# Kernel optimization log

Hardware: AMD Instinct MI355X
Metric: run time of the kernel (lower is better)

## Reference

```python
import jax, jax.numpy as jnp
import numpy as np
import math

B, T, D_MODEL, N_HEADS = 2, 2048, 2048, 16
D_HEAD = D_MODEL // N_HEADS
ROPE_THETA = 10000.0


def setup_inputs() -> dict:
    key = jax.random.key(0)
    ks = jax.random.split(key, 4)
    x = jax.random.normal(ks[0], (B, T, D_MODEL), dtype=jnp.float32)
    # causal mask: True = masked (matches torch masked_fill semantics)
    mask = jnp.triu(jnp.ones((T, T), dtype=bool), k=1)[None, None]  # [1,1,T,T]
    # rotary freqs: complex freqs_cis = exp(i * t * theta^(-2j/d)) -> cos/sin parts
    inv_freq = 1.0 / (ROPE_THETA ** (jnp.arange(0, D_HEAD, 2, dtype=jnp.float32) / D_HEAD))
    angles = jnp.arange(T, dtype=jnp.float32)[:, None] * inv_freq[None, :]  # [T, D_HEAD//2]
    freqs_cos = jnp.cos(angles)
    freqs_sin = jnp.sin(angles)
    s = 1.0 / math.sqrt(D_MODEL)
    Wqkv = jax.random.normal(ks[1], (D_MODEL, 3 * D_MODEL), dtype=jnp.float32) * s
    bqkv = jnp.zeros((3 * D_MODEL,), dtype=jnp.float32)
    Wproj = jax.random.normal(ks[2], (D_MODEL, D_MODEL), dtype=jnp.float32) * s
    bproj = jnp.zeros((D_MODEL,), dtype=jnp.float32)
    return {"x": x, "mask": mask, "freqs_cos": freqs_cos, "freqs_sin": freqs_sin,
            "Wqkv": Wqkv, "bqkv": bqkv, "Wproj": Wproj, "bproj": bproj}


def _rope(t, cos, sin):
    # t: [B,H,T,D]; cos/sin: [1,1,T,D//2]. Complex multiply on (even, odd) pairs.
    t2 = t.reshape(*t.shape[:-1], -1, 2)
    t_re, t_im = t2[..., 0], t2[..., 1]
    out_re = t_re * cos - t_im * sin
    out_im = t_re * sin + t_im * cos
    return jnp.stack([out_re, out_im], axis=-1).reshape(t.shape)


def reference(x, mask, freqs_cos, freqs_sin, Wqkv, bqkv, Wproj, bproj):
    Bb, Tt, C = x.shape
    qkv = x @ Wqkv + bqkv                                   # [B,T,3C]
    q, k, v = jnp.split(qkv, 3, axis=-1)
    def heads(t):
        return t.reshape(Bb, Tt, N_HEADS, D_HEAD).transpose(0, 2, 1, 3)  # [B,H,T,D]
    q, k, v = heads(q), heads(k), heads(v)
    cos = freqs_cos[None, None]                              # [1,1,T,D//2]
    sin = freqs_sin[None, None]
    q = _rope(q, cos, sin)
    k = _rope(k, cos, sin)
    att = jnp.einsum('bhqd,bhkd->bhqk', q, k) / math.sqrt(D_HEAD)
    att = jnp.where(mask, -jnp.inf, att)
    att = jax.nn.softmax(att, axis=-1)
    # attn_dropout is identity in eval mode
    out = jnp.einsum('bhqk,bhkd->bhqd', att, v)              # [B,H,T,D]
    out = out.transpose(0, 2, 1, 3).reshape(Bb, Tt, C)
    return (out @ Wproj + bproj, k, v)
```

## Files before the change

### kernel.cpp

```cpp
#include <hip/hip_runtime.h>
#include <hip/hip_bf16.h>

#define T_SEQ 2048
#define DM    2048
#define NH    16
#define DH    128
#define NBH   32
#define MROWS 4096

typedef __bf16 bf16x8 __attribute__((ext_vector_type(8)));
typedef __bf16 bf16x4 __attribute__((ext_vector_type(4)));
typedef float  f32x4  __attribute__((ext_vector_type(4)));

#define MFMA16 __builtin_amdgcn_mfma_f32_16x16x32_bf16

__device__ __forceinline__ void async_copy16(const void* g, void* l) {
  __builtin_amdgcn_global_load_lds((const __attribute__((address_space(1))) void*)g,
                                   (__attribute__((address_space(3))) void*)l, 16, 0, 0);
}


__global__ void cast_bf16_k(const float* __restrict__ x, __bf16* __restrict__ xb) {
  int i = (blockIdx.x * 256 + threadIdx.x) * 4;
  float4 v = *reinterpret_cast<const float4*>(x + i);
  bf16x4 o;
  o[0] = (__bf16)v.x; o[1] = (__bf16)v.y; o[2] = (__bf16)v.z; o[3] = (__bf16)v.w;
  *reinterpret_cast<bf16x4*>(xb + i) = o;
}

__global__ void transpose_cast_w(const float* __restrict__ W, __bf16* __restrict__ WT,
                                 int K, int N) {
  __shared__ float tile[32][33];
  int n0 = blockIdx.x * 32, k0 = blockIdx.y * 32;
  int tx = threadIdx.x, ty = threadIdx.y;
  #pragma unroll
  for (int i = 0; i < 4; i++)
    tile[ty + i * 8][tx] = W[(size_t)(k0 + ty + i * 8) * N + n0 + tx];
  __syncthreads();
  #pragma unroll
  for (int i = 0; i < 4; i++)
    WT[(size_t)(n0 + ty + i * 8) * K + k0 + tx] = (__bf16)tile[tx][ty + i * 8];
}

__global__ void transpose_v(const __bf16* __restrict__ Vb, __bf16* __restrict__ Vtb) {
  __shared__ __bf16 tile[32][34];
  int t0 = blockIdx.x * 32, d0 = blockIdx.y * 32, bh = blockIdx.z;
  const __bf16* src = Vb + (size_t)bh * T_SEQ * DH;
  __bf16* dst = Vtb + (size_t)bh * DH * T_SEQ;
  int tx = threadIdx.x, ty = threadIdx.y;
  #pragma unroll
  for (int i = 0; i < 4; i++)
    tile[ty + i * 8][tx] = src[(size_t)(t0 + ty + i * 8) * DH + d0 + tx];
  __syncthreads();
  #pragma unroll
  for (int i = 0; i < 4; i++)
    dst[(size_t)(d0 + ty + i * 8) * T_SEQ + t0 + tx] = tile[tx][ty + i * 8];
}


__device__ __forceinline__ bf16x8 rds(const __bf16* base, int row, int chunk) {
  return *reinterpret_cast<const bf16x8*>(
      reinterpret_cast<const char*>(base) + row * 128 + ((chunk ^ (row & 7)) << 4));
}

__device__ __forceinline__ void stage64(const __bf16* g, int K, int kt, char* lds,
                                        int wave, int lane) {
  #pragma unroll
  for (int j = 0; j < 4; j++) {
    int r = wave * 32 + j * 8 + (lane >> 3);
    int c = lane & 7;
    const char* src = (const char*)g + (size_t)r * (K * 2) + kt * 128 + ((c ^ (r & 7)) << 4);
    async_copy16(src, lds + wave * 4096 + j * 1024);
  }
}

template <int EPI>
__global__ __launch_bounds__(256, 2) void gemm_bt(
    const __bf16* __restrict__ A, const __bf16* __restrict__ Bt, int K,
    const float* __restrict__ bias,
    const float* __restrict__ fcos, const float* __restrict__ fsin,
    __bf16* __restrict__ Qb, __bf16* __restrict__ Kb, __bf16* __restrict__ Vb,
    float* __restrict__ kout, float* __restrict__ vout,
    float* __restrict__ outp) {
  __shared__ __align__(16) char smem[65536];
  const int tid = threadIdx.x, lane = tid & 63, wave = tid >> 6;
  const int hi = lane >> 4, lo = lane & 15;
  const int wm = (wave >> 1) * 64, wn = (wave & 1) * 64;
  const __bf16* Ab = A + (size_t)blockIdx.y * 128 * K;
  const __bf16* Bb = Bt + (size_t)blockIdx.x * 128 * K;
  f32x4 acc[4][4] = {};
  const int NK = K >> 6;

  stage64(Ab, K, 0, smem, wave, lane);
  stage64(Bb, K, 0, smem + 32768, wave, lane);
  __syncthreads();

  for (int t = 0; t < NK; ++t) {
    const int sel = (t & 1) ? 16384 : 0;
    const __bf16* Ac = (const __bf16*)(smem + sel);
    const __bf16* Bc = (const __bf16*)(smem + 32768 + sel);
    if (t + 1 < NK) {
      stage64(Ab, K, t + 1, smem + (sel ^ 16384), wave, lane);
      stage64(Bb, K, t + 1, smem + 32768 + (sel ^ 16384), wave, lane);
    }
    bf16x8 a0[4], b0[4], a1[4], b1[4];
    #pragma unroll
    for (int m = 0; m < 4; ++m) a0[m] = rds(Ac, wm + m * 16 + lo, hi);
    #pragma unroll
    for (int n = 0; n < 4; ++n) b0[n] = rds(Bc, wn + n * 16 + lo, hi);
    __builtin_amdgcn_s_setprio(1);
    #pragma unroll
    for (int m = 0; m < 4; ++m)
      #pragma unroll
      for (int n = 0; n < 4; ++n)
        acc[m][n] = MFMA16(a0[m], b0[n], acc[m][n], 0, 0, 0);
    __builtin_amdgcn_s_setprio(0);
    #pragma unroll
    for (int m = 0; m < 4; ++m) a1[m] = rds(Ac, wm + m * 16 + lo, 4 + hi);
    #pragma unroll
    for (int n = 0; n < 4; ++n) b1[n] = rds(Bc, wn + n * 16 + lo, 4 + hi);
    __builtin_amdgcn_s_setprio(1);
    #pragma unroll
    for (int m = 0; m < 4; ++m)
      #pragma unroll
      for (int n = 0; n < 4; ++n)
        acc[m][n] = MFMA16(a1[m], b1[n], acc[m][n], 0, 0, 0);
    __builtin_amdgcn_s_setprio(0);
    __syncthreads();
  }

  float* sc = (float*)smem;
  const int rl_r = tid >> 3;
  const int cb   = (tid & 7) * 16;
  #pragma unroll
  for (int cc = 0; cc < 4; ++cc) {
    __syncthreads();
    if ((wave >> 1) == (cc >> 1)) {
      #pragma unroll
      for (int mm = 0; mm < 2; ++mm) {
        int m = (cc & 1) * 2 + mm;
        #pragma unroll
        for (int j = 0; j < 4; ++j) {
          int col = wn + j * 16 + lo;
          int rl = mm * 16 + hi * 4;
          #pragma unroll
          for (int r = 0; r < 4; ++r)
            sc[(rl + r) * 132 + col] = acc[m][j][r];
        }
      }
    }
    __syncthreads();
    float v[16];
    #pragma unroll
    for (int q = 0; q < 4; ++q)
      *reinterpret_cast<float4*>(&v[q * 4]) =
          *reinterpret_cast<const float4*>(&sc[rl_r * 132 + cb + q * 4]);
    const int row = blockIdx.y * 128 + cc * 32 + rl_r;
    const int n0  = blockIdx.x * 128 + cb;
    #pragma unroll
    for (int q = 0; q < 4; ++q) {
      float4 bv = *reinterpret_cast<const float4*>(&bias[n0 + q * 4]);
      v[q * 4 + 0] += bv.x; v[q * 4 + 1] += bv.y;
      v[q * 4 + 2] += bv.z; v[q * 4 + 3] += bv.w;
    }
    if (EPI == 1) {
      const int which = n0 >> 11;
      const int wn2 = n0 & 2047, h = wn2 >> 7, d0 = wn2 & 127;
      const int b = row >> 11, tt = row & 2047;
      if (which < 2) {
        const float* cp = fcos + tt * 64 + (d0 >> 1);
        const float* sp = fsin + tt * 64 + (d0 >> 1);
        float4 c0 = *reinterpret_cast<const float4*>(cp);
        float4 c1 = *reinterpret_cast<const float4*>(cp + 4);
        float4 s0 = *reinterpret_cast<const float4*>(sp);
        float4 s1 = *reinterpret_cast<const float4*>(sp + 4);
        float cs[8] = {c0.x, c0.y, c0.z, c0.w, c1.x, c1.y, c1.z, c1.w};
        float sn[8] = {s0.x, s0.y, s0.z, s0.w, s1.x, s1.y, s1.z, s1.w};
        #pragma unroll
        for (int p = 0; p < 8; ++p) {
          float re = v[2 * p], im = v[2 * p + 1];
          v[2 * p]     = re * cs[p] - im * sn[p];
          v[2 * p + 1] = re * sn[p] + im * cs[p];
        }
      }
      size_t base = (((size_t)(b * NH + h)) * T_SEQ + tt) * DH + d0;
      bf16x8 o0, o1;
      #pragma unroll
      for (int p = 0; p < 8; ++p) { o0[p] = (__bf16)v[p]; o1[p] = (__bf16)v[8 + p]; }
      if (which == 0) {
        *reinterpret_cast<bf16x8*>(Qb + base) = o0;
        *reinterpret_cast<bf16x8*>(Qb + base + 8) = o1;
      } else if (which == 1) {
        *reinterpret_cast<bf16x8*>(Kb + base) = o0;
        *reinterpret_cast<bf16x8*>(Kb + base + 8) = o1;
        #pragma unroll
        for (int q = 0; q < 4; ++q)
          *reinterpret_cast<float4*>(kout + base + q * 4) =
              *reinterpret_cast<const float4*>(&v[q * 4]);
      } else {
        *reinterpret_cast<bf16x8*>(Vb + base) = o0;
        *reinterpret_cast<bf16x8*>(Vb + base + 8) = o1;
        #pragma unroll
        for (int q = 0; q < 4; ++q)
          *reinterpret_cast<float4*>(vout + base + q * 4) =
              *reinterpret_cast<const float4*>(&v[q * 4]);
      }
    } else {
      float* op = outp + (size_t)row * DM + n0;
      #pragma unroll
      for (int q = 0; q < 4; ++q)
        *reinterpret_cast<float4*>(op + q * 4) =
            *reinterpret_cast<const float4*>(&v[q * 4]);
    }
  }
}


__device__ __forceinline__ bf16x8 lds_frag(const __bf16* base, int row, int chunk) {
  return *reinterpret_cast<const bf16x8*>(
      reinterpret_cast<const char*>(base) + row * 256 + ((chunk ^ (row & 7)) << 4));
}

template <int NLOADS>
__device__ __forceinline__ void stage256(const __bf16* g, __bf16* lds, int tid) {
  const int wave = tid >> 6, lane = tid & 63;
  #pragma unroll
  for (int j = 0; j < NLOADS; j++) {
    int off = j * 8192 + wave * 1024;
    int r = (off >> 8) + (lane >> 4);
    int c = lane & 15;
    const char* gs = (const char*)g + (size_t)r * 256 + ((c ^ (r & 7)) << 4);
    async_copy16(gs, (char*)lds + off);
  }
}

__device__ __forceinline__ void stage_vt(const __bf16* g, int kt, __bf16* lds, int tid) {
  const int wave = tid >> 6, lane = tid & 63;
  #pragma unroll
  for (int j = 0; j < 2; j++) {
    int off = j * 8192 + wave * 1024;
    int r = (off >> 7) + (lane >> 3);
    int c = lane & 7;
    const char* gs = (const char*)g + (size_t)r * (T_SEQ * 2) + kt * 128 + ((c ^ (r & 7)) << 4);
    async_copy16(gs, (char*)lds + off);
  }
}

__global__ __launch_bounds__(512, 2) void attn_fwd(
    const __bf16* __restrict__ Qb, const __bf16* __restrict__ Kb,
    const __bf16* __restrict__ Vtb, __bf16* __restrict__ att_out) {
  __shared__ __bf16 Qs[128 * 128];
  __shared__ __bf16 Ks[64 * 128];
  __shared__ __bf16 Vts[128 * 64];
  __shared__ __bf16 Ps[8 * 16 * 64];
  const int tid = threadIdx.x, lane = tid & 63, wave = tid >> 6;
  const int hi = lane >> 4, lo = lane & 15;
  const int bh = blockIdx.y, b = bh >> 4, h = bh & 15;
  const __bf16* Qg = Qb + (size_t)bh * T_SEQ * DH;
  const __bf16* Kg = Kb + (size_t)bh * T_SEQ * DH;
  const __bf16* Vg = Vtb + (size_t)bh * DH * T_SEQ;
  const float scale = 0.08838834764831845f;
  const float L2E = 1.4426950408889634f;
  __bf16* Pw = Ps + wave * 1024;

  for (int pass = 0; pass < 2; ++pass) {
    const int qi = pass ? (15 - blockIdx.x) : blockIdx.x;
    const int q0 = qi * 128;
    __syncthreads();
    stage256<4>(Qg + (size_t)q0 * DH, Qs, tid);
    f32x4 oacc[8] = {};
    float m = -3e38f, l = 0.f;
    const int qg = q0 + wave * 16 + lo;
    const int NT = 2 * qi + 2;

    for (int kt = 0; kt < NT; ++kt) {
      __syncthreads();
      stage256<2>(Kg + (size_t)kt * 64 * DH, Ks, tid);
      stage_vt(Vg, kt, Vts, tid);
      __syncthreads();

      f32x4 sacc[4] = {};
      #pragma unroll
      for (int ks = 0; ks < 4; ++ks) {
        bf16x8 bq = lds_frag(Qs, wave * 16 + lo, ks * 4 + hi);
        #pragma unroll
        for (int sf = 0; sf < 4; ++sf) {
          bf16x8 ak = lds_frag(Ks, sf * 16 + lo, ks * 4 + hi);
          sacc[sf] = MFMA16(ak, bq, sacc[sf], 0, 0, 0);
        }
      }
      const bool maskt = (kt * 64 + 63) > (q0 + wave * 16);
      float mx = -3e38f;
      #pragma unroll
      for (int sf = 0; sf < 4; ++sf)
        #pragma unroll
        for (int r = 0; r < 4; ++r) {
          float v = sacc[sf][r] * scale;
          if (maskt && (kt * 64 + sf * 16 + hi * 4 + r) > qg) v = -3e38f;
          sacc[sf][r] = v;
          mx = fmaxf(mx, v);
        }
      mx = fmaxf(mx, __shfl_xor(mx, 16, 64));
      mx = fmaxf(mx, __shfl_xor(mx, 32, 64));
      const bool nr = __all(mx - m <= 8.0f);
      if (!nr) {
        float mnew = fmaxf(m, mx);
        float alpha = __builtin_exp2f((m - mnew) * L2E);
        m = mnew;
        l *= alpha;
        #pragma unroll
        for (int df = 0; df < 8; ++df) {
          oacc[df][0] *= alpha; oacc[df][1] *= alpha;
          oacc[df][2] *= alpha; oacc[df][3] *= alpha;
        }
      }
      float rs = 0.f;
      #pragma unroll
      for (int sf = 0; sf < 4; ++sf)
        #pragma unroll
        for (int r = 0; r < 4; ++r) {
          float p = __builtin_exp2f((sacc[sf][r] - m) * L2E);
          sacc[sf][r] = p;
          rs += p;
        }
      rs += __shfl_xor(rs, 16, 64);
      rs += __shfl_xor(rs, 32, 64);
      l += rs;
      #pragma unroll
      for (int sf = 0; sf < 4; ++sf) {
        bf16x4 pk;
        pk[0] = (__bf16)sacc[sf][0]; pk[1] = (__bf16)sacc[sf][1];
        pk[2] = (__bf16)sacc[sf][2]; pk[3] = (__bf16)sacc[sf][3];
        int byte = sf * 32 + hi * 8;
        int chunk = byte >> 4, rem = byte & 15;
        char* p = (char*)Pw + lo * 128 + (((chunk ^ (lo & 7)) << 4) | rem);
        *reinterpret_cast<bf16x4*>(p) = pk;
      }
      #pragma unroll
      for (int ks = 0; ks < 2; ++ks) {
        bf16x8 bp = rds(Pw, lo, ks * 4 + hi);
        #pragma unroll
        for (int df = 0; df < 8; ++df) {
          bf16x8 av = rds(Vts, df * 16 + lo, ks * 4 + hi);
          oacc[df] = MFMA16(av, bp, oacc[df], 0, 0, 0);
        }
      }
    }

    float inv = 1.0f / l;
    int qrow = b * T_SEQ + q0 + wave * 16 + lo;
    #pragma unroll
    for (int df = 0; df < 8; ++df) {
      bf16x4 pk;
      pk[0] = (__bf16)(oacc[df][0] * inv);
      pk[1] = (__bf16)(oacc[df][1] * inv);
      pk[2] = (__bf16)(oacc[df][2] * inv);
      pk[3] = (__bf16)(oacc[df][3] * inv);
      int d = df * 16 + hi * 4;
      *reinterpret_cast<bf16x4*>(att_out + (size_t)qrow * DM + h * DH + d) = pk;
    }
  }
}


extern "C" void kernel_launch(void* const* d_in, const int* in_sizes, int n_in,
                              void* d_out, int out_size, void* d_ws, size_t ws_size,
                              hipStream_t stream) {
  const float* x     = (const float*)d_in[0];
  const float* fcos  = (const float*)d_in[2];
  const float* fsin  = (const float*)d_in[3];
  const float* Wqkv  = (const float*)d_in[4];
  const float* bqkv  = (const float*)d_in[5];
  const float* Wproj = (const float*)d_in[6];
  const float* bproj = (const float*)d_in[7];
  float* out  = (float*)d_out;
  float* kout = out + (size_t)8388608;
  float* vout = out + (size_t)16777216;

  char* ws = (char*)d_ws;
  __bf16* xb     = (__bf16*)(ws);
  __bf16* WqkvT  = (__bf16*)(ws + 16777216);
  __bf16* WprojT = (__bf16*)(ws + 41943040);
  __bf16* Qb     = (__bf16*)(ws + 50331648);
  __bf16* Kb     = (__bf16*)(ws + 67108864);
  __bf16* Vb     = (__bf16*)(ws + 83886080);
  __bf16* Vtb    = (__bf16*)(ws + 100663296);
  __bf16* att    = xb;

  cast_bf16_k<<<8192, 256, 0, stream>>>(x, xb);
  transpose_cast_w<<<dim3(192, 64), dim3(32, 8), 0, stream>>>(Wqkv, WqkvT, DM, 3 * DM);
  transpose_cast_w<<<dim3(64, 64), dim3(32, 8), 0, stream>>>(Wproj, WprojT, DM, DM);
  gemm_bt<1><<<dim3(48, 32), 256, 0, stream>>>(xb, WqkvT, DM, bqkv, fcos, fsin,
                                               Qb, Kb, Vb, kout, vout, nullptr);
  transpose_v<<<dim3(64, 4, NBH), dim3(32, 8), 0, stream>>>(Vb, Vtb);
  attn_fwd<<<dim3(8, NBH), 512, 0, stream>>>(Qb, Kb, Vtb, att);
  gemm_bt<0><<<dim3(16, 32), 256, 0, stream>>>(att, WprojT, DM, bproj, nullptr, nullptr,
                                               nullptr, nullptr, nullptr, nullptr, nullptr, out);
}
```

Measured before the change: 301.0 us.

## Shrink attention blocks to 64 queries, register-resident Q, XCD-aware grid

The attention kernel now uses 256-thread blocks covering 64 query rows instead of 512 threads covering 128, and launches 512 blocks on a 1D grid. Each block still processes a mirrored pair of query tiles to balance causal work. The grid index is remapped so that heads are grouped per XCD for L2 locality of K/V. Q fragments are loaded directly into registers instead of staged through LDS, masking is applied only on the diagonal tile, and s_setprio raises wave priority around the MFMA loops. The aim is better occupancy and load balance across CUs at the cost of less K/V reuse per block.

```diff
diff --git a/kernel.cpp b/kernel.cpp
--- a/kernel.cpp
+++ b/kernel.cpp
@@ -221,12 +221,11 @@
       reinterpret_cast<const char*>(base) + row * 256 + ((chunk ^ (row & 7)) << 4));
 }
 
-template <int NLOADS>
-__device__ __forceinline__ void stage256(const __bf16* g, __bf16* lds, int tid) {
+__device__ __forceinline__ void stage64x256(const __bf16* g, __bf16* lds, int tid) {
   const int wave = tid >> 6, lane = tid & 63;
   #pragma unroll
-  for (int j = 0; j < NLOADS; j++) {
-    int off = j * 8192 + wave * 1024;
+  for (int j = 0; j < 4; j++) {
+    int off = j * 4096 + wave * 1024;
     int r = (off >> 8) + (lane >> 4);
     int c = lane & 15;
     const char* gs = (const char*)g + (size_t)r * 256 + ((c ^ (r & 7)) << 4);
@@ -234,28 +233,32 @@
   }
 }
 
-__device__ __forceinline__ void stage_vt(const __bf16* g, int kt, __bf16* lds, int tid) {
+__device__ __forceinline__ void stage128x128(const __bf16* g, size_t rstrideB, int colB,
+                                             __bf16* lds, int tid) {
   const int wave = tid >> 6, lane = tid & 63;
   #pragma unroll
-  for (int j = 0; j < 2; j++) {
-    int off = j * 8192 + wave * 1024;
+  for (int j = 0; j < 4; j++) {
+    int off = j * 4096 + wave * 1024;
     int r = (off >> 7) + (lane >> 3);
     int c = lane & 7;
-    const char* gs = (const char*)g + (size_t)r * (T_SEQ * 2) + kt * 128 + ((c ^ (r & 7)) << 4);
+    const char* gs = (const char*)g + (size_t)r * rstrideB + colB + ((c ^ (r & 7)) << 4);
     async_copy16(gs, (char*)lds + off);
   }
 }
 
-__global__ __launch_bounds__(512, 2) void attn_fwd(
+__global__ __launch_bounds__(256, 2) void attn_fwd(
     const __bf16* __restrict__ Qb, const __bf16* __restrict__ Kb,
     const __bf16* __restrict__ Vtb, __bf16* __restrict__ att_out) {
-  __shared__ __bf16 Qs[128 * 128];
   __shared__ __bf16 Ks[64 * 128];
   __shared__ __bf16 Vts[128 * 64];
-  __shared__ __bf16 Ps[8 * 16 * 64];
+  __shared__ __bf16 Ps[4 * 16 * 64];
   const int tid = threadIdx.x, lane = tid & 63, wave = tid >> 6;
   const int hi = lane >> 4, lo = lane & 15;
-  const int bh = blockIdx.y, b = bh >> 4, h = bh & 15;
+  const int linear = (int)blockIdx.x;
+  const int xcd = linear & 7, rest = linear >> 3;
+  const int bh = xcd + 8 * (rest >> 4);
+  const int pair = rest & 15;
+  const int b = bh >> 4, h = bh & 15;
   const __bf16* Qg = Qb + (size_t)bh * T_SEQ * DH;
   const __bf16* Kg = Kb + (size_t)bh * T_SEQ * DH;
   const __bf16* Vg = Vtb + (size_t)bh * DH * T_SEQ;
@@ -264,39 +267,41 @@
   __bf16* Pw = Ps + wave * 1024;
 
   for (int pass = 0; pass < 2; ++pass) {
-    const int qi = pass ? (15 - blockIdx.x) : blockIdx.x;
-    const int q0 = qi * 128;
-    __syncthreads();
-    stage256<4>(Qg + (size_t)q0 * DH, Qs, tid);
+    const int qj = pass ? (31 - pair) : pair;
+    const int q0 = qj * 64;
+    const int qg = q0 + wave * 16 + lo;
+    bf16x8 qf[4];
+    const __bf16* qp = Qg + (size_t)qg * DH + hi * 8;
+    #pragma unroll
+    for (int ks = 0; ks < 4; ++ks) qf[ks] = *reinterpret_cast<const bf16x8*>(qp + ks * 32);
     f32x4 oacc[8] = {};
     float m = -3e38f, l = 0.f;
-    const int qg = q0 + wave * 16 + lo;
-    const int NT = 2 * qi + 2;
+    const int NT = qj + 1;
 
     for (int kt = 0; kt < NT; ++kt) {
       __syncthreads();
-      stage256<2>(Kg + (size_t)kt * 64 * DH, Ks, tid);
-      stage_vt(Vg, kt, Vts, tid);
+      stage64x256(Kg + (size_t)kt * 64 * DH, Ks, tid);
+      stage128x128(Vg, (size_t)T_SEQ * 2, kt * 128, Vts, tid);
       __syncthreads();
 
       f32x4 sacc[4] = {};
-      #pragma unroll
-      for (int ks = 0; ks < 4; ++ks) {
-        bf16x8 bq = lds_frag(Qs, wave * 16 + lo, ks * 4 + hi);
+      __builtin_amdgcn_s_setprio(1);
+      #pragma unroll
+      for (int ks = 0; ks < 4; ++ks)
         #pragma unroll
         for (int sf = 0; sf < 4; ++sf) {
           bf16x8 ak = lds_frag(Ks, sf * 16 + lo, ks * 4 + hi);
-          sacc[sf] = MFMA16(ak, bq, sacc[sf], 0, 0, 0);
-        }
-      }
-      const bool maskt = (kt * 64 + 63) > (q0 + wave * 16);
+          sacc[sf] = MFMA16(ak, qf[ks], sacc[sf], 0, 0, 0);
+        }
+      __builtin_amdgcn_s_setprio(0);
+      const bool diag = (kt == NT - 1);
       float mx = -3e38f;
       #pragma unroll
       for (int sf = 0; sf < 4; ++sf)
         #pragma unroll
         for (int r = 0; r < 4; ++r) {
           float v = sacc[sf][r] * scale;
-          if (maskt && (kt * 64 + sf * 16 + hi * 4 + r) > qg) v = -3e38f;
+          if (diag && (kt * 64 + sf * 16 + hi * 4 + r) > qg) v = -3e38f;
           sacc[sf][r] = v;
           mx = fmaxf(mx, v);
         }
@@ -336,6 +341,7 @@
         char* p = (char*)Pw + lo * 128 + (((chunk ^ (lo & 7)) << 4) | rem);
         *reinterpret_cast<bf16x4*>(p) = pk;
       }
+      __builtin_amdgcn_s_setprio(1);
       #pragma unroll
       for (int ks = 0; ks < 2; ++ks) {
         bf16x8 bp = rds(Pw, lo, ks * 4 + hi);
@@ -345,6 +351,7 @@
           oacc[df] = MFMA16(av, bp, oacc[df], 0, 0, 0);
         }
       }
+      __builtin_amdgcn_s_setprio(0);
     }
 
     float inv = 1.0f / l;
@@ -393,7 +400,7 @@
   gemm_bt<1><<<dim3(48, 32), 256, 0, stream>>>(xb, WqkvT, DM, bqkv, fcos, fsin,
                                                Qb, Kb, Vb, kout, vout, nullptr);
   transpose_v<<<dim3(64, 4, NBH), dim3(32, 8), 0, stream>>>(Vb, Vtb);
-  attn_fwd<<<dim3(8, NBH), 512, 0, stream>>>(Qb, Kb, Vtb, att);
+  attn_fwd<<<512, 256, 0, stream>>>(Qb, Kb, Vtb, att);
   gemm_bt<0><<<dim3(16, 32), 256, 0, stream>>>(att, WprojT, DM, bproj, nullptr, nullptr,
                                                nullptr, nullptr, nullptr, nullptr, nullptr, out);
 }
```

New measurement: 281.6 us. 6.4% less time.
